# Performance work log

Measured on AMD Instinct MI355X. Metric: run time of the kernel, lower is better.

Reference implementation:

```python
import jax, jax.numpy as jnp
import numpy as np

PAD_IDX = 0
K = 5
TEMPERATURE = 1.0
BATCH = 256
VOCAB = 50257


def setup_inputs() -> dict:
    key = jax.random.key(0)
    k1, k2, k3, k4, k5 = jax.random.split(key, 5)
    draft_tokens = jax.random.randint(k1, (BATCH, K), 0, VOCAB)
    # valid-ish log-probabilities (negative values)
    draft_log_probs = -jax.random.uniform(k2, (BATCH, K), minval=0.05, maxval=8.0, dtype=jnp.float32)
    target_logits = jax.random.normal(k3, (BATCH, K, VOCAB), dtype=jnp.float32)
    random_vals = jax.random.uniform(k4, (BATCH, K), dtype=jnp.float32)
    uniform_sample = jax.random.uniform(k5, (BATCH,), dtype=jnp.float32)
    return {
        "draft_tokens": draft_tokens,
        "draft_log_probs": draft_log_probs,
        "target_logits": target_logits,
        "random_vals": random_vals,
        "uniform_sample": uniform_sample,
    }


def reference(draft_tokens, draft_log_probs, target_logits, random_vals, uniform_sample):
    B, k = draft_tokens.shape
    # --- accept/reject scan ---
    tlp = jax.nn.log_softmax(target_logits / TEMPERATURE, axis=-1)          # [B,k,V]
    tlp_draft = jnp.take_along_axis(tlp, draft_tokens[..., None], axis=2)[..., 0]  # [B,k]
    accept_probs = jnp.minimum(jnp.exp(tlp_draft - draft_log_probs), 1.0)
    accepted_mask = random_vals < accept_probs
    rejected_sent = jnp.concatenate(
        [~accepted_mask, jnp.ones((B, 1), dtype=bool)], axis=1)              # [B,k+1]
    first_reject = jnp.argmax(rejected_sent, axis=1)                         # [B]
    n_accepted = first_reject
    # fixed-width (k) accepted_tokens, PAD-filled past n_accepted (jit-friendly
    # variant of torch's dynamic max_accepted truncation; same valid entries)
    pos = jnp.arange(k)[None, :]
    accepted_tokens = jnp.where(pos < n_accepted[:, None], draft_tokens, PAD_IDX)
    # --- vectorized fallback sampling at first reject position ---
    rp = jnp.minimum(first_reject, k - 1)                                    # clamp for gather
    sel_logits = jnp.take_along_axis(target_logits, rp[:, None, None], axis=1)[:, 0, :]  # [B,V]
    target_probs = jax.nn.softmax(sel_logits / TEMPERATURE, axis=-1)
    dlp_sel = jnp.take_along_axis(draft_log_probs, rp[:, None], axis=1)      # [B,1]
    # torch builds a constant vector exp(dlp) over the whole vocab
    draft_probs = jnp.exp(dlp_sel)                                           # [B,1] broadcasts
    adjusted = jnp.clip(target_probs - draft_probs, 0.0)
    s = adjusted.sum(axis=-1, keepdims=True)
    probs = jnp.where(s > 0, adjusted / jnp.where(s > 0, s, 1.0), target_probs)  # [B,V]
    # multinomial(probs, 1) via inverse CDF with provided uniform sample
    cdf = jnp.cumsum(probs, axis=-1)
    thresh = uniform_sample[:, None] * cdf[:, -1:]
    sampled = jnp.argmax(cdf >= thresh, axis=-1)                             # [B]
    final_tokens = jnp.where(first_reject < k, sampled, PAD_IDX)
    return accepted_tokens, n_accepted, final_tokens
```

## Files before the change

### kernel.cpp

```cpp
#include <hip/hip_runtime.h>
#include <math.h>
#include <stdint.h>

#define VOCAB 50257
#define KD 5
#define NBATCH 256
#define NT 1024
#define NW (NT / 64)
#define NTILES ((VOCAB + NT - 1) / NT)

__global__ __launch_bounds__(NT) void spec_decode_kernel(
    const int* __restrict__ dtok,
    const float* __restrict__ dlp,
    const float* __restrict__ logits,
    const float* __restrict__ rnd,
    const float* __restrict__ usmp,
    int* __restrict__ out)
{
    const int b    = blockIdx.x;
    const int tid  = threadIdx.x;
    const int lane = tid & 63;
    const int wv   = tid >> 6;

    __shared__ double s_w[NW];
    __shared__ double s_tileA[NTILES];
    __shared__ double s_tileR[NTILES];
    __shared__ double s_dbc[2];
    __shared__ int    s_ibc[2];
    __shared__ int    s_found;

    double Zsel  = 0.0;
    int    n_acc = KD;
    for (int r = 0; r < KD; ++r) {
        const float* row = logits + ((size_t)b * KD + r) * (size_t)VOCAB;
        int head = (int)((4u - ((((uintptr_t)row) >> 2) & 3u)) & 3u);
        double local = 0.0;
        if (tid < head) local += (double)expf(row[tid]);
        int nvec = (VOCAB - head) >> 2;
        const float4* row4 = (const float4*)(row + head);
        for (int i = tid; i < nvec; i += NT) {
            float4 x = row4[i];
            local += (double)expf(x.x) + (double)expf(x.y)
                   + (double)expf(x.z) + (double)expf(x.w);
        }
        int tail_start = head + (nvec << 2);
        int tail_cnt   = VOCAB - tail_start;
        if (tid < tail_cnt) local += (double)expf(row[tail_start + tid]);

        for (int off = 32; off; off >>= 1) local += __shfl_down(local, off, 64);
        if (lane == 0) s_w[wv] = local;
        __syncthreads();
        if (tid == 0) {
            double Z = 0.0;
            for (int w = 0; w < NW; ++w) Z += s_w[w];
            int    tok  = dtok[b * KD + r];
            double tlp  = (double)row[tok] - log(Z);
            double ap   = exp(tlp - (double)dlp[b * KD + r]);
            if (ap > 1.0) ap = 1.0;
            s_dbc[0] = Z;
            s_ibc[0] = ((double)rnd[b * KD + r] < ap) ? 1 : 0;
        }
        __syncthreads();
        Zsel = s_dbc[0];
        int acc = s_ibc[0];
        __syncthreads();
        if (!acc) { n_acc = r; break; }
    }

    if (tid == 0) {
        for (int r = 0; r < KD; ++r)
            out[b * KD + r] = (r < n_acc) ? dtok[b * KD + r] : 0;
        out[NBATCH * KD + b] = n_acc;
        if (n_acc >= KD) out[NBATCH * KD + NBATCH + b] = 0;
        s_found = 0x7FFFFFFF;
    }
    if (n_acc >= KD) return;

    const int    rp   = n_acc;
    const float* row  = logits + ((size_t)b * KD + rp) * (size_t)VOCAB;
    const double invZ = 1.0 / Zsel;
    const double dp   = exp((double)dlp[b * KD + rp]);

    for (int t = wv; t < NTILES; t += NW) {
        double aS = 0.0, rS = 0.0;
        int base = t * NT;
        for (int j = 0; j < NT / 64; ++j) {
            int idx = base + j * 64 + lane;
            if (idx < VOCAB) {
                double p = exp((double)row[idx]) * invZ;
                rS += p;
                double a = p - dp;
                if (a > 0.0) aS += a;
            }
        }
        for (int off = 32; off; off >>= 1) {
            aS += __shfl_down(aS, off, 64);
            rS += __shfl_down(rS, off, 64);
        }
        if (lane == 0) { s_tileA[t] = aS; s_tileR[t] = rS; }
    }
    __syncthreads();

    if (tid == 0) {
        double S = 0.0;
        for (int t = 0; t < NTILES; ++t) S += s_tileA[t];
        int useAdj = (S > 0.0) ? 1 : 0;
        double Tot = S;
        if (!useAdj) {
            Tot = 0.0;
            for (int t = 0; t < NTILES; ++t) Tot += s_tileR[t];
        }
        double T = (double)usmp[b] * Tot;
        const double* tiles = useAdj ? s_tileA : s_tileR;
        double P = 0.0;
        int    ct = NTILES - 1;
        for (int t = 0; t < NTILES; ++t) {
            if (P + tiles[t] >= T || t == NTILES - 1) { ct = t; break; }
            P += tiles[t];
        }
        s_dbc[0] = P;
        s_dbc[1] = T;
        s_ibc[0] = ct;
        s_ibc[1] = useAdj;
    }
    __syncthreads();

    {
        double Pb     = s_dbc[0];
        double T      = s_dbc[1];
        int    ct     = s_ibc[0];
        int    useAdj = s_ibc[1];
        int    idx    = ct * NT + tid;
        double g      = 0.0;
        if (idx < VOCAB) {
            double p = exp((double)row[idx]) * invZ;
            if (useAdj) {
                double a = p - dp;
                g = (a > 0.0) ? a : 0.0;
            } else {
                g = p;
            }
        }
        double sc = g;
        for (int off = 1; off < 64; off <<= 1) {
            double v = __shfl_up(sc, (unsigned)off, 64);
            if (lane >= off) sc += v;
        }
        if (lane == 63) s_w[wv] = sc;
        __syncthreads();
        double woff = 0.0;
        for (int w = 0; w < wv; ++w) woff += s_w[w];
        double incl = Pb + woff + sc;
        if (idx < VOCAB && incl >= T) atomicMin(&s_found, idx);
        __syncthreads();
        if (tid == 0) {
            int smp = s_found;
            if (smp == 0x7FFFFFFF) {
                smp = ct * NT + NT - 1;
                if (smp > VOCAB - 1) smp = VOCAB - 1;
            }
            out[NBATCH * KD + NBATCH + b] = smp;
        }
    }
}

extern "C" void kernel_launch(void* const* d_in, const int* in_sizes, int n_in,
                              void* d_out, int out_size, void* d_ws, size_t ws_size,
                              hipStream_t stream) {
    const int*   dtok   = (const int*)d_in[0];
    const float* dlp    = (const float*)d_in[1];
    const float* logits = (const float*)d_in[2];
    const float* rnd    = (const float*)d_in[3];
    const float* usmp   = (const float*)d_in[4];
    int*         out    = (int*)d_out;
    (void)in_sizes; (void)n_in; (void)out_size; (void)d_ws; (void)ws_size;
    spec_decode_kernel<<<dim3(NBATCH), dim3(NT), 0, stream>>>(
        dtok, dlp, logits, rnd, usmp, out);
}
```

Measured before the change: 341.8 us.

## Split row-0 softmax normalizer into a separate wide-grid pre-kernel

Adds a first kernel that computes the row-0 exp-sum for every batch, split across 8 segments per batch (2048 blocks of 256 threads), and writes partial sums to the workspace. The main kernel then reads and sums these partials for r=0 instead of streaming the first row itself. The aim is to spread the always-needed first-row reduction across more blocks than the 256-block grid can fill. The cost is an extra launch, and the workspace is assumed to be large enough.

```diff
diff --git a/kernel.cpp b/kernel.cpp
--- a/kernel.cpp
+++ b/kernel.cpp
@@ -5,16 +5,61 @@
 #define VOCAB 50257
 #define KD 5
 #define NBATCH 256
-#define NT 1024
-#define NW (NT / 64)
-#define NTILES ((VOCAB + NT - 1) / NT)
-
-__global__ __launch_bounds__(NT) void spec_decode_kernel(
+#define NSPLIT 8
+#define SEG ((VOCAB + NSPLIT - 1) / NSPLIT)
+#define NT1 256
+#define NT2 1024
+#define NW2 (NT2 / 64)
+#define NTILES ((VOCAB + NT2 - 1) / NT2)
+
+__global__ __launch_bounds__(NT1) void zsum_row0_kernel(
+    const float* __restrict__ logits, double* __restrict__ part)
+{
+    const int bid = blockIdx.x;
+    const int b   = bid / NSPLIT;
+    const int seg = bid % NSPLIT;
+    const int tid = threadIdx.x;
+    const int lane = tid & 63, wv = tid >> 6;
+
+    const float* row = logits + (size_t)b * KD * (size_t)VOCAB;
+    int s0 = seg * SEG;
+    int s1 = s0 + SEG; if (s1 > VOCAB) s1 = VOCAB;
+    const float* p = row + s0;
+    int n = s1 - s0;
+
+    int head = (int)((4u - ((((uintptr_t)p) >> 2) & 3u)) & 3u);
+    if (head > n) head = n;
+    double local = 0.0;
+    if (tid < head) local += (double)expf(p[tid]);
+    int nvec = (n - head) >> 2;
+    const float4* p4 = (const float4*)(p + head);
+    for (int i = tid; i < nvec; i += NT1) {
+        float4 x = p4[i];
+        local += (double)expf(x.x) + (double)expf(x.y)
+               + (double)expf(x.z) + (double)expf(x.w);
+    }
+    int ts = head + (nvec << 2);
+    int tc = n - ts;
+    if (tid < tc) local += (double)expf(p[ts + tid]);
+
+    for (int off = 32; off; off >>= 1) local += __shfl_down(local, off, 64);
+    __shared__ double sw[NT1 / 64];
+    if (lane == 0) sw[wv] = local;
+    __syncthreads();
+    if (tid == 0) {
+        double Z = 0.0;
+        for (int w = 0; w < NT1 / 64; ++w) Z += sw[w];
+        part[bid] = Z;
+    }
+}
+
+__global__ __launch_bounds__(NT2) void decide_sample_kernel(
     const int* __restrict__ dtok,
     const float* __restrict__ dlp,
     const float* __restrict__ logits,
     const float* __restrict__ rnd,
     const float* __restrict__ usmp,
+    const double* __restrict__ part,
     int* __restrict__ out)
 {
     const int b    = blockIdx.x;
@@ -22,7 +67,7 @@
     const int lane = tid & 63;
     const int wv   = tid >> 6;
 
-    __shared__ double s_w[NW];
+    __shared__ double s_w[NW2];
     __shared__ double s_tileA[NTILES];
     __shared__ double s_tileR[NTILES];
     __shared__ double s_dbc[2];
@@ -33,31 +78,43 @@
     int    n_acc = KD;
     for (int r = 0; r < KD; ++r) {
         const float* row = logits + ((size_t)b * KD + r) * (size_t)VOCAB;
-        int head = (int)((4u - ((((uintptr_t)row) >> 2) & 3u)) & 3u);
-        double local = 0.0;
-        if (tid < head) local += (double)expf(row[tid]);
-        int nvec = (VOCAB - head) >> 2;
-        const float4* row4 = (const float4*)(row + head);
-        for (int i = tid; i < nvec; i += NT) {
-            float4 x = row4[i];
-            local += (double)expf(x.x) + (double)expf(x.y)
-                   + (double)expf(x.z) + (double)expf(x.w);
-        }
-        int tail_start = head + (nvec << 2);
-        int tail_cnt   = VOCAB - tail_start;
-        if (tid < tail_cnt) local += (double)expf(row[tail_start + tid]);
-
-        for (int off = 32; off; off >>= 1) local += __shfl_down(local, off, 64);
-        if (lane == 0) s_w[wv] = local;
-        __syncthreads();
+        if (r > 0) {
+            int head = (int)((4u - ((((uintptr_t)row) >> 2) & 3u)) & 3u);
+            double local = 0.0;
+            if (tid < head) local += (double)expf(row[tid]);
+            int nvec = (VOCAB - head) >> 2;
+            const float4* row4 = (const float4*)(row + head);
+            for (int i = tid; i < nvec; i += NT2) {
+                float4 x = row4[i];
+                local += (double)expf(x.x) + (double)expf(x.y)
+                       + (double)expf(x.z) + (double)expf(x.w);
+            }
+            int ts = head + (nvec << 2);
+            int tc = VOCAB - ts;
+            if (tid < tc) local += (double)expf(row[ts + tid]);
+            for (int off = 32; off; off >>= 1) local += __shfl_down(local, off, 64);
+            if (lane == 0) s_w[wv] = local;
+            __syncthreads();
+            if (tid == 0) {
+                double Z = 0.0;
+                for (int w = 0; w < NW2; ++w) Z += s_w[w];
+                s_dbc[0] = Z;
+            }
+            __syncthreads();
+        } else {
+            if (tid == 0) {
+                double Z = 0.0;
+                for (int s = 0; s < NSPLIT; ++s) Z += part[b * NSPLIT + s];
+                s_dbc[0] = Z;
+            }
+            __syncthreads();
+        }
         if (tid == 0) {
-            double Z = 0.0;
-            for (int w = 0; w < NW; ++w) Z += s_w[w];
-            int    tok  = dtok[b * KD + r];
-            double tlp  = (double)row[tok] - log(Z);
-            double ap   = exp(tlp - (double)dlp[b * KD + r]);
+            double Z   = s_dbc[0];
+            int    tok = dtok[b * KD + r];
+            double tlp = (double)row[tok] - log(Z);
+            double ap  = exp(tlp - (double)dlp[b * KD + r]);
             if (ap > 1.0) ap = 1.0;
-            s_dbc[0] = Z;
             s_ibc[0] = ((double)rnd[b * KD + r] < ap) ? 1 : 0;
         }
         __syncthreads();
@@ -81,10 +138,10 @@
     const double invZ = 1.0 / Zsel;
     const double dp   = exp((double)dlp[b * KD + rp]);
 
-    for (int t = wv; t < NTILES; t += NW) {
+    for (int t = wv; t < NTILES; t += NW2) {
         double aS = 0.0, rS = 0.0;
-        int base = t * NT;
-        for (int j = 0; j < NT / 64; ++j) {
+        int base = t * NT2;
+        for (int j = 0; j < NT2 / 64; ++j) {
             int idx = base + j * 64 + lane;
             if (idx < VOCAB) {
                 double p = exp((double)row[idx]) * invZ;
@@ -130,7 +187,7 @@
         double T      = s_dbc[1];
         int    ct     = s_ibc[0];
         int    useAdj = s_ibc[1];
-        int    idx    = ct * NT + tid;
+        int    idx    = ct * NT2 + tid;
         double g      = 0.0;
         if (idx < VOCAB) {
             double p = exp((double)row[idx]) * invZ;
@@ -156,7 +213,7 @@
         if (tid == 0) {
             int smp = s_found;
             if (smp == 0x7FFFFFFF) {
-                smp = ct * NT + NT - 1;
+                smp = ct * NT2 + NT2 - 1;
                 if (smp > VOCAB - 1) smp = VOCAB - 1;
             }
             out[NBATCH * KD + NBATCH + b] = smp;
@@ -173,7 +230,10 @@
     const float* rnd    = (const float*)d_in[3];
     const float* usmp   = (const float*)d_in[4];
     int*         out    = (int*)d_out;
-    (void)in_sizes; (void)n_in; (void)out_size; (void)d_ws; (void)ws_size;
-    spec_decode_kernel<<<dim3(NBATCH), dim3(NT), 0, stream>>>(
-        dtok, dlp, logits, rnd, usmp, out);
+    double*      part   = (double*)d_ws;
+    (void)in_sizes; (void)n_in; (void)out_size; (void)ws_size;
+
+    zsum_row0_kernel<<<dim3(NBATCH * NSPLIT), dim3(NT1), 0, stream>>>(logits, part);
+    decide_sample_kernel<<<dim3(NBATCH), dim3(NT2), 0, stream>>>(
+        dtok, dlp, logits, rnd, usmp, part, out);
 }
```

Measured after the change: 347.4 us. No clear change (+1.7%).
